# Performance work log

Measured on AMD Instinct MI355X. Metric: run time of the kernel, lower is better.

Reference implementation:

```python
import jax, jax.numpy as jnp
import numpy as np

D = 512      # d_model
H = 8        # n_heads
HD = D // H  # head_dim = 64
PS = 4       # patch_size
B, T, P = 4, 4096, 1024


def setup_inputs() -> dict:
    key = jax.random.key(0)
    ks = jax.random.split(key, 12)
    s = 1.0 / np.sqrt(D)
    return {
        "token_hidden": jax.random.normal(ks[0], (B, T, D), jnp.float32),
        "patch_hidden": jax.random.normal(ks[1], (B, P, D), jnp.float32),
        "Wq": jax.random.normal(ks[2], (D, D), jnp.float32) * s,
        "Wk": jax.random.normal(ks[3], (D, D), jnp.float32) * s,
        "Wv": jax.random.normal(ks[4], (D, D), jnp.float32) * s,
        "bq": jax.random.normal(ks[5], (D,), jnp.float32) * 0.02,
        "bk": jax.random.normal(ks[6], (D,), jnp.float32) * 0.02,
        "bv": jax.random.normal(ks[7], (D,), jnp.float32) * 0.02,
        "Wo": jax.random.normal(ks[8], (D, D), jnp.float32) * s,
        "bo": jax.random.normal(ks[9], (D,), jnp.float32) * 0.02,
    }


def reference(token_hidden, patch_hidden, Wq, Wk, Wv, bq, bk, bv, Wo, bo):
    b, t, _ = token_hidden.shape
    p = patch_hidden.shape[1]
    # QKV projections (equivalent to nn.MultiheadAttention in_proj)
    q = (token_hidden @ Wq + bq).reshape(b, t, H, HD)
    k = (patch_hidden @ Wk + bk).reshape(b, p, H, HD)
    v = (patch_hidden @ Wv + bv).reshape(b, p, H, HD)
    # scaled dot-product scores: [b, h, t, p]
    scores = jnp.einsum('bthd,bphd->bhtp', q, k) / jnp.sqrt(jnp.asarray(HD, q.dtype))
    # block-causal token-to-patch mask: token i attends to patches 0..i//PS
    allowed = jnp.arange(p)[None, :] <= (jnp.arange(t)[:, None] // PS)  # [t, p]
    scores = jnp.where(allowed[None, None, :, :], scores, -jnp.inf)
    attn = jax.nn.softmax(scores, axis=-1)
    ctx = jnp.einsum('bhtp,bphd->bthd', attn, v).reshape(b, t, D)
    out = ctx @ Wo + bo  # out_proj
    return token_hidden + out
```

## Files before the change

### kernel.cpp

```cpp
#include <hip/hip_runtime.h>
#include <stdint.h>

#define DM 512
#define NH 8
#define HDIM 64
#define TT 4096
#define PP 1024

typedef float f32x4 __attribute__((ext_vector_type(4)));
typedef __bf16 bf16x8 __attribute__((ext_vector_type(8)));
typedef unsigned short u16x8 __attribute__((ext_vector_type(8)));
typedef unsigned short u16x4 __attribute__((ext_vector_type(4)));
typedef unsigned int u32x2 __attribute__((ext_vector_type(2)));
typedef unsigned int u32x4 __attribute__((ext_vector_type(4)));

static __device__ __forceinline__ unsigned short f2bf(float f) {
  unsigned u = __builtin_bit_cast(unsigned, f);
  u += 0x7fff + ((u >> 16) & 1);
  return (unsigned short)(u >> 16);
}

static __device__ __forceinline__ unsigned packtr(float a, float b) {
  return __builtin_amdgcn_perm(__builtin_bit_cast(unsigned, b),
                               __builtin_bit_cast(unsigned, a), 0x07060302u);
}

static __device__ __forceinline__ float fexp2(float x) {
#if __has_builtin(__builtin_amdgcn_exp2f)
  return __builtin_amdgcn_exp2f(x);
#else
  return __expf(x * 0.69314718055994531f);
#endif
}

static __device__ __forceinline__ void load_lds16(const void* g, void* l) {
  __builtin_amdgcn_global_load_lds(
      (__attribute__((address_space(1))) void*)g,
      (__attribute__((address_space(3))) void*)l, 16, 0, 0);
}

static __device__ __forceinline__ f32x4 mfma16(bf16x8 a, bf16x8 b, f32x4 c) {
  return __builtin_amdgcn_mfma_f32_16x16x32_bf16(a, b, c, 0, 0, 0);
}

static __device__ __forceinline__ bf16x8 p_exchange(unsigned w0, unsigned w1,
                                                    unsigned w2, unsigned w3,
                                                    int q, int c) {
#if __has_builtin(__builtin_amdgcn_permlane32_swap) && \
    __has_builtin(__builtin_amdgcn_permlane16_swap)
  (void)q; (void)c;
  auto s02 = __builtin_amdgcn_permlane32_swap(w0, w2, false, false);
  auto t02 = __builtin_amdgcn_permlane16_swap(s02[0], s02[1], false, false);
  auto s13 = __builtin_amdgcn_permlane32_swap(w1, w3, false, false);
  auto t13 = __builtin_amdgcn_permlane16_swap(s13[0], s13[1], false, false);
  u32x4 pd = {(unsigned)t02[0], (unsigned)t13[0], (unsigned)t02[1], (unsigned)t13[1]};
  return __builtin_bit_cast(bf16x8, pd);
#else
  const int a0 = (c + (q & 1) * 32) * 4;
  const int a2 = (c + 16 + (q & 1) * 32) * 4;
  const bool lo = (q < 2);
  unsigned d0 = lo ? (unsigned)__builtin_amdgcn_ds_bpermute(a0, (int)w0)
                   : (unsigned)__builtin_amdgcn_ds_bpermute(a0, (int)w2);
  unsigned d1 = lo ? (unsigned)__builtin_amdgcn_ds_bpermute(a0, (int)w1)
                   : (unsigned)__builtin_amdgcn_ds_bpermute(a0, (int)w3);
  unsigned d2 = lo ? (unsigned)__builtin_amdgcn_ds_bpermute(a2, (int)w0)
                   : (unsigned)__builtin_amdgcn_ds_bpermute(a2, (int)w2);
  unsigned d3 = lo ? (unsigned)__builtin_amdgcn_ds_bpermute(a2, (int)w1)
                   : (unsigned)__builtin_amdgcn_ds_bpermute(a2, (int)w3);
  u32x4 pd = {d0, d1, d2, d3};
  return __builtin_bit_cast(bf16x8, pd);
#endif
}

__global__ __launch_bounds__(256) void k_conv(
    const float* __restrict__ tok, const float* __restrict__ pat,
    const float* __restrict__ wq, const float* __restrict__ wk,
    const float* __restrict__ wv, const float* __restrict__ wo,
    unsigned short* __restrict__ xtok, unsigned short* __restrict__ xpat,
    unsigned short* __restrict__ wt) {
  const int gid = blockIdx.x * 256 + threadIdx.x;
  const int NX = 2621440;
  if (gid < NX) {
    int i4 = gid * 4;
    const float* src;
    unsigned short* dst;
    int idx;
    if (i4 < 8388608) { src = tok; dst = xtok; idx = i4; }
    else              { src = pat; dst = xpat; idx = i4 - 8388608; }
    f32x4 v = *(const f32x4*)&src[idx];
    u16x4 o;
#pragma unroll
    for (int i = 0; i < 4; ++i) o[i] = f2bf(v[i]);
    *(u16x4*)&dst[idx] = o;
  } else {
    int wi = gid - NX;
    int wid = wi >> 16;
    int e = (wi & 65535) << 2;
    int k = e >> 9, n = e & 511;
    const float* w = (wid == 0) ? wq : (wid == 1) ? wk : (wid == 2) ? wv : wo;
    f32x4 v = *(const f32x4*)&w[e];
    unsigned short* wtb = wt + (wid << 18);
#pragma unroll
    for (int i = 0; i < 4; ++i) wtb[(n + i) * 512 + k] = f2bf(v[i]);
  }
}

template <int MODE>
__device__ __forceinline__ void gemm_bf16_body(
    const unsigned short* __restrict__ A, const unsigned short* __restrict__ Wt,
    const float* __restrict__ bias, unsigned short* __restrict__ outb,
    int bid, unsigned short* sA, unsigned short* sB, float scale) {
  const int tid = threadIdx.x;
  const int wave = tid >> 6, lane = tid & 63;
  const int q = lane >> 4, c = lane & 15;
  const int bm = bid >> 2, bn = bid & 3;
  const int wm = (wave >> 1) * 64, wn = (wave & 1) * 64;
  const int lr = lane >> 2, lc = (lane & 3) * 8;

  f32x4 acc[4][4];
#pragma unroll
  for (int i = 0; i < 4; ++i)
#pragma unroll
    for (int j = 0; j < 4; ++j) acc[i][j] = (f32x4){0.f, 0.f, 0.f, 0.f};

  const int rowA0 = bm * 128, rowB0 = bn * 128;

  auto stage = [&](int t) {
    const int kn = t * 32;
    unsigned short* dA = sA + (t % 3) * 4096;
    unsigned short* dB = sB + (t % 3) * 4096;
#pragma unroll
    for (int qq = 0; qq < 2; ++qq) {
      const int chunk = wave * 2 + qq;
      load_lds16(&A[(rowA0 + chunk * 16 + lr) * 512 + kn + lc], &dA[chunk * 512]);
      load_lds16(&Wt[(rowB0 + chunk * 16 + lr) * 512 + kn + lc], &dB[chunk * 512]);
    }
  };

  stage(0);
  stage(1);
  asm volatile("s_waitcnt vmcnt(4)" ::: "memory");
  __builtin_amdgcn_s_barrier();

#pragma unroll 1
  for (int i = 0; i < 16; ++i) {
    if (i + 2 < 16) stage(i + 2);
    const unsigned short* curA = sA + (i % 3) * 4096;
    const unsigned short* curB = sB + (i % 3) * 4096;
    bf16x8 af[4], bfr[4];
#pragma unroll
    for (int mt = 0; mt < 4; ++mt)
      af[mt] = __builtin_bit_cast(bf16x8, *(const u16x8*)&curA[(wm + mt * 16 + c) * 32 + q * 8]);
#pragma unroll
    for (int nt = 0; nt < 4; ++nt)
      bfr[nt] = __builtin_bit_cast(bf16x8, *(const u16x8*)&curB[(wn + nt * 16 + c) * 32 + q * 8]);
#pragma unroll
    for (int mt = 0; mt < 4; ++mt)
#pragma unroll
      for (int nt = 0; nt < 4; ++nt) {
        if (MODE == 2)
          acc[mt][nt] = mfma16(af[mt], bfr[nt], acc[mt][nt]);
        else
          acc[mt][nt] = mfma16(bfr[nt], af[mt], acc[mt][nt]);
      }
    if (i < 15) {
      if (i + 2 < 16) asm volatile("s_waitcnt vmcnt(4)" ::: "memory");
      else            asm volatile("s_waitcnt vmcnt(0)" ::: "memory");
      __builtin_amdgcn_s_barrier();
    }
  }

  if (MODE == 2) {
#pragma unroll
    for (int nt = 0; nt < 4; ++nt) {
      const int col = bn * 128 + wn + nt * 16 + c;
      const float bcol = bias[col];
#pragma unroll
      for (int mt = 0; mt < 4; ++mt) {
        const int row0 = bm * 128 + wm + mt * 16 + q * 4;
        u16x4 o;
#pragma unroll
        for (int r = 0; r < 4; ++r) o[r] = f2bf(acc[mt][nt][r] + bcol);
        *(u16x4*)&outb[((row0 >> 10) << 19) + (col << 10) + (row0 & 1023)] = o;
      }
    }
  } else {
#pragma unroll
    for (int mt = 0; mt < 4; ++mt) {
      const int row = bm * 128 + wm + mt * 16 + c;
#pragma unroll
      for (int nt = 0; nt < 4; ++nt) {
        const int col0 = bn * 128 + wn + nt * 16 + q * 4;
        const f32x4 bv = *(const f32x4*)&bias[col0];
        u16x4 o;
#pragma unroll
        for (int r = 0; r < 4; ++r) o[r] = f2bf((acc[mt][nt][r] + bv[r]) * scale);
        *(u16x4*)&outb[row * 512 + col0] = o;
      }
    }
  }
}

__global__ __launch_bounds__(256) void k_gemm_qkv(
    const unsigned short* __restrict__ xtok, const unsigned short* __restrict__ xpat,
    const unsigned short* __restrict__ WT,
    const float* __restrict__ bq, const float* __restrict__ bk,
    const float* __restrict__ bv,
    unsigned short* __restrict__ QB, unsigned short* __restrict__ KB,
    unsigned short* __restrict__ VTB) {
  __shared__ unsigned short sA[3 * 128 * 32];
  __shared__ unsigned short sB[3 * 128 * 32];
  const int bid = blockIdx.x;
  if (bid < 512) {
    gemm_bf16_body<0>(xtok, WT, bq, QB, bid, sA, sB, 0.18033688011112042f);
  } else if (bid < 640) {
    gemm_bf16_body<1>(xpat, WT + 262144, bk, KB, bid - 512, sA, sB, 1.0f);
  } else {
    gemm_bf16_body<2>(xpat, WT + 524288, bv, VTB, bid - 640, sA, sB, 1.0f);
  }
}

__global__ __launch_bounds__(256) void k_gemm_o(
    const unsigned short* __restrict__ A, const unsigned short* __restrict__ Wt,
    const float* __restrict__ bias, float* __restrict__ outf,
    const float* __restrict__ resid) {
  __shared__ unsigned short sA[3 * 128 * 32];
  __shared__ unsigned short sB[3 * 128 * 32];
  const int tid = threadIdx.x;
  const int wave = tid >> 6, lane = tid & 63;
  const int q = lane >> 4, c = lane & 15;
  const int bm = blockIdx.x >> 2, bn = blockIdx.x & 3;
  const int wm = (wave >> 1) * 64, wn = (wave & 1) * 64;
  const int lr = lane >> 2, lc = (lane & 3) * 8;

  f32x4 acc[4][4];
#pragma unroll
  for (int i = 0; i < 4; ++i)
#pragma unroll
    for (int j = 0; j < 4; ++j) acc[i][j] = (f32x4){0.f, 0.f, 0.f, 0.f};

  const int rowA0 = bm * 128, rowB0 = bn * 128;

  auto stage = [&](int t) {
    const int kn = t * 32;
    unsigned short* dA = sA + (t % 3) * 4096;
    unsigned short* dB = sB + (t % 3) * 4096;
#pragma unroll
    for (int qq = 0; qq < 2; ++qq) {
      const int chunk = wave * 2 + qq;
      load_lds16(&A[(rowA0 + chunk * 16 + lr) * 512 + kn + lc], &dA[chunk * 512]);
      load_lds16(&Wt[(rowB0 + chunk * 16 + lr) * 512 + kn + lc], &dB[chunk * 512]);
    }
  };

  stage(0);
  stage(1);
  asm volatile("s_waitcnt vmcnt(4)" ::: "memory");
  __builtin_amdgcn_s_barrier();

#pragma unroll 1
  for (int i = 0; i < 16; ++i) {
    if (i + 2 < 16) stage(i + 2);
    const unsigned short* curA = sA + (i % 3) * 4096;
    const unsigned short* curB = sB + (i % 3) * 4096;
    bf16x8 af[4], bfr[4];
#pragma unroll
    for (int mt = 0; mt < 4; ++mt)
      af[mt] = __builtin_bit_cast(bf16x8, *(const u16x8*)&curA[(wm + mt * 16 + c) * 32 + q * 8]);
#pragma unroll
    for (int nt = 0; nt < 4; ++nt)
      bfr[nt] = __builtin_bit_cast(bf16x8, *(const u16x8*)&curB[(wn + nt * 16 + c) * 32 + q * 8]);
#pragma unroll
    for (int mt = 0; mt < 4; ++mt)
#pragma unroll
      for (int nt = 0; nt < 4; ++nt)
        acc[mt][nt] = mfma16(bfr[nt], af[mt], acc[mt][nt]);
    if (i < 15) {
      if (i + 2 < 16) asm volatile("s_waitcnt vmcnt(4)" ::: "memory");
      else            asm volatile("s_waitcnt vmcnt(0)" ::: "memory");
      __builtin_amdgcn_s_barrier();
    }
  }

#pragma unroll
  for (int mt = 0; mt < 4; ++mt) {
    const int row = bm * 128 + wm + mt * 16 + c;
#pragma unroll
    for (int nt = 0; nt < 4; ++nt) {
      const int col0 = bn * 128 + wn + nt * 16 + q * 4;
      const int o = row * 512 + col0;
      const f32x4 bv = *(const f32x4*)&bias[col0];
      const f32x4 rv = *(const f32x4*)&resid[o];
      f32x4 ov;
#pragma unroll
      for (int r = 0; r < 4; ++r) ov[r] = acc[mt][nt][r] + bv[r] + rv[r];
      *(f32x4*)&outf[o] = ov;
    }
  }
}

__global__ __launch_bounds__(256) void k_attn(
    const unsigned short* __restrict__ Q,
    const unsigned short* __restrict__ K,
    const unsigned short* __restrict__ VT,
    unsigned short* __restrict__ CTX) {
  __shared__ unsigned short sK[2][32 * 88];
  __shared__ unsigned short sV[2][64 * 40];

  const int tid = threadIdx.x;
  const int lane = tid & 63;
  const int wave = tid >> 6;
  const int q = lane >> 4, c = lane & 15;

  const int g = blockIdx.x >> 5;
  const int tg = (g < 16) ? g : 47 - g;
  const int bh = blockIdx.x & 31;
  const int b = bh >> 3, h = bh & 7;
  const int t0 = tg * 128 + wave * 32;
  const int tA = t0 + c, tB = t0 + 16 + c;

  const int qbA = (b * TT + tA) * 512 + h * 64 + q * 8;
  const int qbB = (b * TT + tB) * 512 + h * 64 + q * 8;
  const bf16x8 qfA0 = __builtin_bit_cast(bf16x8, *(const u16x8*)&Q[qbA]);
  const bf16x8 qfA1 = __builtin_bit_cast(bf16x8, *(const u16x8*)&Q[qbA + 32]);
  const bf16x8 qfB0 = __builtin_bit_cast(bf16x8, *(const u16x8*)&Q[qbB]);
  const bf16x8 qfB1 = __builtin_bit_cast(bf16x8, *(const u16x8*)&Q[qbB + 32]);

  f32x4 oA[4], oB[4];
#pragma unroll
  for (int m = 0; m < 4; ++m) {
    oA[m] = (f32x4){0.f, 0.f, 0.f, 0.f};
    oB[m] = (f32x4){0.f, 0.f, 0.f, 0.f};
  }
  f32x4 lA = (f32x4){0.f, 0.f, 0.f, 0.f};
  f32x4 lB = lA;
  const u16x8 onesu = {0x3F80, 0x3F80, 0x3F80, 0x3F80, 0x3F80, 0x3F80, 0x3F80, 0x3F80};
  const bf16x8 ones = __builtin_bit_cast(bf16x8, onesu);

  const int ntile = tg + 1;
  const int krow = tid >> 3, kcol = (tid & 7) * 8;
  const int vrow = tid >> 2, vcol = (tid & 3) * 8;
  const int kg = (b * PP + krow) * 512 + h * 64 + kcol;
  const int vg = (b << 19) + ((h * 64 + vrow) << 10) + vcol;

  u16x8 kreg = *(const u16x8*)&K[kg];
  u16x8 vreg = *(const u16x8*)&VT[vg];
  *(u16x8*)&sK[0][krow * 88 + kcol] = kreg;
  *(u16x8*)&sV[0][vrow * 40 + vcol] = vreg;
  __syncthreads();

#pragma unroll 1
  for (int pt = 0; pt < ntile; ++pt) {
    const int buf = pt & 1;
    const bool more = (pt + 1 < ntile);
    if (more) {
      kreg = *(const u16x8*)&K[kg + (pt + 1) * 32 * 512];
      vreg = *(const u16x8*)&VT[vg + (pt + 1) * 32];
    }
    const unsigned short* bK = sK[buf];
    const unsigned short* bV = sV[buf];

    const bf16x8 ka0 = __builtin_bit_cast(bf16x8, *(const u16x8*)&bK[c * 88 + q * 8]);
    const bf16x8 ka1 = __builtin_bit_cast(bf16x8, *(const u16x8*)&bK[c * 88 + 32 + q * 8]);
    const bf16x8 kb0 = __builtin_bit_cast(bf16x8, *(const u16x8*)&bK[(16 + c) * 88 + q * 8]);
    const bf16x8 kb1 = __builtin_bit_cast(bf16x8, *(const u16x8*)&bK[(16 + c) * 88 + 32 + q * 8]);

    const f32x4 z = (f32x4){0.f, 0.f, 0.f, 0.f};
    __builtin_amdgcn_s_setprio(1);
    f32x4 sA0 = mfma16(ka1, qfA1, mfma16(ka0, qfA0, z));
    f32x4 sA1 = mfma16(kb1, qfA1, mfma16(kb0, qfA0, z));
    f32x4 sB0 = mfma16(ka1, qfB1, mfma16(ka0, qfB0, z));
    f32x4 sB1 = mfma16(kb1, qfB1, mfma16(kb0, qfB0, z));
    __builtin_amdgcn_s_setprio(0);

    if (pt + 1 == ntile) {
      const int p0 = pt * 32;
      const int limA = tA >> 2, limB = tB >> 2;
      const int pb0 = p0 + q * 4, pb1 = p0 + 16 + q * 4;
#pragma unroll
      for (int r = 0; r < 4; ++r) {
        if (pb0 + r > limA) sA0[r] = -1e30f;
        if (pb1 + r > limA) sA1[r] = -1e30f;
        if (pb0 + r > limB) sB0[r] = -1e30f;
        if (pb1 + r > limB) sB1[r] = -1e30f;
      }
    }

    float pA0[4], pA1[4], pB0[4], pB1[4];
#pragma unroll
    for (int r = 0; r < 4; ++r) {
      pA0[r] = fexp2(sA0[r]);
      pA1[r] = fexp2(sA1[r]);
      pB0[r] = fexp2(sB0[r]);
      pB1[r] = fexp2(sB1[r]);
    }

    const bf16x8 pbA = p_exchange(packtr(pA0[0], pA0[1]), packtr(pA0[2], pA0[3]),
                                  packtr(pA1[0], pA1[1]), packtr(pA1[2], pA1[3]), q, c);
    const bf16x8 pbB = p_exchange(packtr(pB0[0], pB0[1]), packtr(pB0[2], pB0[3]),
                                  packtr(pB1[0], pB1[1]), packtr(pB1[2], pB1[3]), q, c);

    __builtin_amdgcn_s_setprio(1);
#pragma unroll
    for (int mt = 0; mt < 4; ++mt) {
      const bf16x8 vf =
          __builtin_bit_cast(bf16x8, *(const u16x8*)&bV[(mt * 16 + c) * 40 + q * 8]);
      oA[mt] = mfma16(vf, pbA, oA[mt]);
      oB[mt] = mfma16(vf, pbB, oB[mt]);
    }
    lA = mfma16(ones, pbA, lA);
    lB = mfma16(ones, pbB, lB);
    __builtin_amdgcn_s_setprio(0);

    if (more) {
      *(u16x8*)&sK[buf ^ 1][krow * 88 + kcol] = kreg;
      *(u16x8*)&sV[buf ^ 1][vrow * 40 + vcol] = vreg;
      __syncthreads();
    }
  }

  const float invA = 1.f / lA[0];
  const float invB = 1.f / lB[0];
  const int obA = (b * TT + tA) * 512 + h * 64 + q * 4;
  const int obB = (b * TT + tB) * 512 + h * 64 + q * 4;
#pragma unroll
  for (int mt = 0; mt < 4; ++mt) {
    u16x4 oa, ob;
#pragma unroll
    for (int r = 0; r < 4; ++r) {
      oa[r] = f2bf(oA[mt][r] * invA);
      ob[r] = f2bf(oB[mt][r] * invB);
    }
    *(u16x4*)&CTX[obA + mt * 16] = oa;
    *(u16x4*)&CTX[obB + mt * 16] = ob;
  }
}

extern "C" void kernel_launch(void* const* d_in, const int* in_sizes, int n_in,
                              void* d_out, int out_size, void* d_ws, size_t ws_size,
                              hipStream_t stream) {
  const float* tok = (const float*)d_in[0];
  const float* pat = (const float*)d_in[1];
  const float* Wq = (const float*)d_in[2];
  const float* Wk = (const float*)d_in[3];
  const float* Wv = (const float*)d_in[4];
  const float* bq = (const float*)d_in[5];
  const float* bk = (const float*)d_in[6];
  const float* bv = (const float*)d_in[7];
  const float* Wo = (const float*)d_in[8];
  const float* bo = (const float*)d_in[9];
  float* out = (float*)d_out;

  unsigned short* ws = (unsigned short*)d_ws;
  unsigned short* WT = ws;
  unsigned short* XTOK = ws + 1048576;
  unsigned short* XPAT = ws + 9437184;
  unsigned short* QB = ws + 11534336;
  unsigned short* KB = ws + 19922944;
  unsigned short* VTB = ws + 22020096;
  unsigned short* CTX = ws + 24117248;

  k_conv<<<11264, 256, 0, stream>>>(tok, pat, Wq, Wk, Wv, Wo, XTOK, XPAT, WT);
  k_gemm_qkv<<<768, 256, 0, stream>>>(XTOK, XPAT, WT, bq, bk, bv, QB, KB, VTB);
  k_attn<<<1024, 256, 0, stream>>>(QB, KB, VTB, CTX);
  k_gemm_o<<<512, 256, 0, stream>>>(CTX, WT + 786432, bo, out, tok);
}
```

Baseline: 195.1 us.

## Fuse fp32-to-bf16 activation conversion into QKV GEMM A-tile loading

Drops the separate pass that converted the token and patch activations to bf16 in workspace. The QKV GEMM now loads fp32 A tiles into registers, converts them to bf16 and writes them to a double-buffered LDS tile, while the B tile keeps its async LDS loads. This removes one full read and write of the activations plus a kernel launch. In exchange the GEMM reads twice as many bytes for A, uses more registers per thread, and adds an LDS write and wait step inside the main loop.

```diff
diff --git a/kernel.cpp b/kernel.cpp
--- a/kernel.cpp
+++ b/kernel.cpp
@@ -9,6 +9,7 @@
 
 typedef float f32x4 __attribute__((ext_vector_type(4)));
 typedef __bf16 bf16x8 __attribute__((ext_vector_type(8)));
+typedef __bf16 bf16x4 __attribute__((ext_vector_type(4)));
 typedef unsigned short u16x8 __attribute__((ext_vector_type(8)));
 typedef unsigned short u16x4 __attribute__((ext_vector_type(4)));
 typedef unsigned int u32x2 __attribute__((ext_vector_type(2)));
@@ -72,42 +73,24 @@
 #endif
 }
 
-__global__ __launch_bounds__(256) void k_conv(
-    const float* __restrict__ tok, const float* __restrict__ pat,
+__global__ __launch_bounds__(256) void k_convW(
     const float* __restrict__ wq, const float* __restrict__ wk,
     const float* __restrict__ wv, const float* __restrict__ wo,
-    unsigned short* __restrict__ xtok, unsigned short* __restrict__ xpat,
     unsigned short* __restrict__ wt) {
-  const int gid = blockIdx.x * 256 + threadIdx.x;
-  const int NX = 2621440;
-  if (gid < NX) {
-    int i4 = gid * 4;
-    const float* src;
-    unsigned short* dst;
-    int idx;
-    if (i4 < 8388608) { src = tok; dst = xtok; idx = i4; }
-    else              { src = pat; dst = xpat; idx = i4 - 8388608; }
-    f32x4 v = *(const f32x4*)&src[idx];
-    u16x4 o;
-#pragma unroll
-    for (int i = 0; i < 4; ++i) o[i] = f2bf(v[i]);
-    *(u16x4*)&dst[idx] = o;
-  } else {
-    int wi = gid - NX;
-    int wid = wi >> 16;
-    int e = (wi & 65535) << 2;
-    int k = e >> 9, n = e & 511;
-    const float* w = (wid == 0) ? wq : (wid == 1) ? wk : (wid == 2) ? wv : wo;
-    f32x4 v = *(const f32x4*)&w[e];
-    unsigned short* wtb = wt + (wid << 18);
-#pragma unroll
-    for (int i = 0; i < 4; ++i) wtb[(n + i) * 512 + k] = f2bf(v[i]);
-  }
+  const int wi = blockIdx.x * 256 + threadIdx.x;
+  int wid = wi >> 16;
+  int e = (wi & 65535) << 2;
+  int k = e >> 9, n = e & 511;
+  const float* w = (wid == 0) ? wq : (wid == 1) ? wk : (wid == 2) ? wv : wo;
+  f32x4 v = *(const f32x4*)&w[e];
+  unsigned short* wtb = wt + (wid << 18);
+#pragma unroll
+  for (int i = 0; i < 4; ++i) wtb[(n + i) * 512 + k] = f2bf(v[i]);
 }
 
 template <int MODE>
-__device__ __forceinline__ void gemm_bf16_body(
-    const unsigned short* __restrict__ A, const unsigned short* __restrict__ Wt,
+__device__ __forceinline__ void gemm_qkv_body(
+    const float* __restrict__ A, const unsigned short* __restrict__ Wt,
     const float* __restrict__ bias, unsigned short* __restrict__ outb,
     int bid, unsigned short* sA, unsigned short* sB, float scale) {
   const int tid = threadIdx.x;
@@ -125,27 +108,55 @@
 
   const int rowA0 = bm * 128, rowB0 = bn * 128;
 
-  auto stage = [&](int t) {
+  f32x4 rA0[2][2], rA1[2][2];
+
+  auto a_issue = [&](int t, f32x4 (&r)[2][2]) {
     const int kn = t * 32;
-    unsigned short* dA = sA + (t % 3) * 4096;
+#pragma unroll
+    for (int qq = 0; qq < 2; ++qq) {
+      const float* src = &A[(rowA0 + (wave * 2 + qq) * 16 + lr) * 512 + kn + lc];
+      r[qq][0] = *(const f32x4*)src;
+      r[qq][1] = *(const f32x4*)(src + 4);
+    }
+  };
+  auto a_write = [&](int t, f32x4 (&r)[2][2]) {
+    unsigned short* dA = sA + (t & 1) * 4096;
+#pragma unroll
+    for (int qq = 0; qq < 2; ++qq) {
+      u16x4 lo = __builtin_bit_cast(u16x4, __builtin_convertvector(r[qq][0], bf16x4));
+      u16x4 hi = __builtin_bit_cast(u16x4, __builtin_convertvector(r[qq][1], bf16x4));
+      u16x8 o = {lo[0], lo[1], lo[2], lo[3], hi[0], hi[1], hi[2], hi[3]};
+      *(u16x8*)&dA[(wave * 2 + qq) * 512 + lr * 32 + lc] = o;
+    }
+  };
+  auto b_issue = [&](int t) {
+    const int kn = t * 32;
     unsigned short* dB = sB + (t % 3) * 4096;
 #pragma unroll
     for (int qq = 0; qq < 2; ++qq) {
       const int chunk = wave * 2 + qq;
-      load_lds16(&A[(rowA0 + chunk * 16 + lr) * 512 + kn + lc], &dA[chunk * 512]);
       load_lds16(&Wt[(rowB0 + chunk * 16 + lr) * 512 + kn + lc], &dB[chunk * 512]);
     }
   };
 
-  stage(0);
-  stage(1);
-  asm volatile("s_waitcnt vmcnt(4)" ::: "memory");
+  a_issue(0, rA0);
+  b_issue(0);
+  a_issue(1, rA1);
+  b_issue(1);
+  asm volatile("s_waitcnt vmcnt(6)" ::: "memory");
+  a_write(0, rA0);
+  asm volatile("s_waitcnt lgkmcnt(0)" ::: "memory");
   __builtin_amdgcn_s_barrier();
 
 #pragma unroll 1
   for (int i = 0; i < 16; ++i) {
-    if (i + 2 < 16) stage(i + 2);
-    const unsigned short* curA = sA + (i % 3) * 4096;
+    const bool ev = ((i & 1) == 0);
+    if (i + 2 < 16) {
+      if (ev) a_issue(i + 2, rA0);
+      else    a_issue(i + 2, rA1);
+      b_issue(i + 2);
+    }
+    const unsigned short* curA = sA + (i & 1) * 4096;
     const unsigned short* curB = sB + (i % 3) * 4096;
     bf16x8 af[4], bfr[4];
 #pragma unroll
@@ -164,8 +175,11 @@
           acc[mt][nt] = mfma16(bfr[nt], af[mt], acc[mt][nt]);
       }
     if (i < 15) {
-      if (i + 2 < 16) asm volatile("s_waitcnt vmcnt(4)" ::: "memory");
-      else            asm volatile("s_waitcnt vmcnt(0)" ::: "memory");
+      if (i < 14) asm volatile("s_waitcnt vmcnt(6)" ::: "memory");
+      else        asm volatile("s_waitcnt vmcnt(0)" ::: "memory");
+      if (ev) a_write(i + 1, rA1);
+      else    a_write(i + 1, rA0);
+      asm volatile("s_waitcnt lgkmcnt(0)" ::: "memory");
       __builtin_amdgcn_s_barrier();
     }
   }
@@ -201,22 +215,22 @@
   }
 }
 
-__global__ __launch_bounds__(256) void k_gemm_qkv(
-    const unsigned short* __restrict__ xtok, const unsigned short* __restrict__ xpat,
+__global__ __launch_bounds__(256, 3) void k_gemm_qkv(
+    const float* __restrict__ tok, const float* __restrict__ pat,
     const unsigned short* __restrict__ WT,
     const float* __restrict__ bq, const float* __restrict__ bk,
     const float* __restrict__ bv,
     unsigned short* __restrict__ QB, unsigned short* __restrict__ KB,
     unsigned short* __restrict__ VTB) {
-  __shared__ unsigned short sA[3 * 128 * 32];
+  __shared__ unsigned short sA[2 * 128 * 32];
   __shared__ unsigned short sB[3 * 128 * 32];
   const int bid = blockIdx.x;
   if (bid < 512) {
-    gemm_bf16_body<0>(xtok, WT, bq, QB, bid, sA, sB, 0.18033688011112042f);
+    gemm_qkv_body<0>(tok, WT, bq, QB, bid, sA, sB, 0.18033688011112042f);
   } else if (bid < 640) {
-    gemm_bf16_body<1>(xpat, WT + 262144, bk, KB, bid - 512, sA, sB, 1.0f);
+    gemm_qkv_body<1>(pat, WT + 262144, bk, KB, bid - 512, sA, sB, 1.0f);
   } else {
-    gemm_bf16_body<2>(xpat, WT + 524288, bv, VTB, bid - 640, sA, sB, 1.0f);
+    gemm_qkv_body<2>(pat, WT + 524288, bv, VTB, bid - 640, sA, sB, 1.0f);
   }
 }
 
@@ -453,15 +467,13 @@
 
   unsigned short* ws = (unsigned short*)d_ws;
   unsigned short* WT = ws;
-  unsigned short* XTOK = ws + 1048576;
-  unsigned short* XPAT = ws + 9437184;
   unsigned short* QB = ws + 11534336;
   unsigned short* KB = ws + 19922944;
   unsigned short* VTB = ws + 22020096;
   unsigned short* CTX = ws + 24117248;
 
-  k_conv<<<11264, 256, 0, stream>>>(tok, pat, Wq, Wk, Wv, Wo, XTOK, XPAT, WT);
-  k_gemm_qkv<<<768, 256, 0, stream>>>(XTOK, XPAT, WT, bq, bk, bv, QB, KB, VTB);
+  k_convW<<<1024, 256, 0, stream>>>(Wq, Wk, Wv, Wo, WT);
+  k_gemm_qkv<<<768, 256, 0, stream>>>(tok, pat, WT, bq, bk, bv, QB, KB, VTB);
   k_attn<<<1024, 256, 0, stream>>>(QB, KB, VTB, CTX);
   k_gemm_o<<<512, 256, 0, stream>>>(CTX, WT + 786432, bo, out, tok);
 }
```

Result: no change. 195.1 us (+0.0%).
